# Performance work log

Measured on AMD Instinct MI355X. Metric: run time of the kernel, lower is better.

Reference implementation:

```python
import jax, jax.numpy as jnp
import numpy as np

BITS = 4
GROUP_SIZE = 128
IN_FEATURES = 4096
OUT_FEATURES = 14336
M = 256  # rows of x; >= kernel_switch_threshold so torch takes the dequant+matmul path


def setup_inputs() -> dict:
    key = jax.random.key(0)
    k1, k2, k3, k4 = jax.random.split(key, 4)
    x = jax.random.normal(k1, (M, IN_FEATURES), dtype=jnp.float16)
    # packed int4 weights: in_features//32*bits rows of int32
    qweight = jax.random.randint(
        k2, (IN_FEATURES // 32 * BITS, OUT_FEATURES), 0, 2**31 - 1, dtype=jnp.int32
    )
    n_groups = IN_FEATURES // GROUP_SIZE
    scales = jax.random.uniform(k3, (n_groups, OUT_FEATURES), dtype=jnp.float32) * 0.01 + 0.001
    # note: module stores zeros as scale*zero product (see pack()); any float works
    zeros = jax.random.uniform(k4, (n_groups, OUT_FEATURES), dtype=jnp.float32) * 0.05
    return {"x": x, "qweight": qweight, "scales": scales, "zeros": zeros}


def reference(x, qweight, scales, zeros):
    # Unpack 8 int4 values from each int32 (little-endian nibbles), matching
    # torch: (qweight[:,None,:] >> wf) & 0xF with wf = [0,4,...,28].
    shifts = jnp.arange(0, 32, BITS, dtype=jnp.int32)          # [8]
    w = (qweight[:, None, :] >> shifts[None, :, None]) & (2**BITS - 1)  # [K/8, 8, N]
    w = w.reshape(-1, GROUP_SIZE, qweight.shape[1])             # [n_groups, group, N]
    s = scales.astype(jnp.float16)[:, None, :]                  # [n_groups, 1, N]
    z = zeros.astype(jnp.float16)[:, None, :]
    # group-wise asymmetric dequant: scale * q - (scale*zero)
    w = (s * w.astype(jnp.float16) - z).reshape(-1, qweight.shape[1])  # [K, N]
    out = jnp.matmul(x, w)                                      # [M, N] fp16
    return out.astype(x.dtype)
```

## Files before the change

### kernel.cpp

```cpp
#include <hip/hip_runtime.h>
#include <hip/hip_fp16.h>

typedef unsigned int u32;
typedef unsigned short u16;
typedef __attribute__((ext_vector_type(8))) _Float16 f16x8;
typedef __attribute__((ext_vector_type(4))) float f32x4;
typedef __attribute__((ext_vector_type(4))) u32 u32x4;

#define M_DIM 256
#define K_DIM 4096
#define N_DIM 14336
#define BM 64
#define BN 128
#define BK 64
#define KHALF (K_DIM / 2)
#define NITER (KHALF / BK)
#define NBLK 896
#define LDA 72

union U4F8 { u32x4 u; f16x8 v; };

__device__ __forceinline__ f16x8 dq8(u32 q, __half2 s2, __half2 d2, __half2 z2) {
  const u32 q1 = q >> 4, q2 = q >> 8, q3 = q >> 12;
  U4F8 r;
  const u32 x0 = ( q & 0x000F000Fu) | 0x64006400u;
  const u32 x1 = (q1 & 0x000F000Fu) | 0x64006400u;
  const u32 x2 = (q2 & 0x000F000Fu) | 0x64006400u;
  const u32 x3 = (q3 & 0x000F000Fu) | 0x64006400u;
  r.u.x = __builtin_bit_cast(u32, __hsub2(__hfma2(__builtin_bit_cast(__half2, x0), s2, d2), z2));
  r.u.y = __builtin_bit_cast(u32, __hsub2(__hfma2(__builtin_bit_cast(__half2, x1), s2, d2), z2));
  r.u.z = __builtin_bit_cast(u32, __hsub2(__hfma2(__builtin_bit_cast(__half2, x2), s2, d2), z2));
  r.u.w = __builtin_bit_cast(u32, __hsub2(__hfma2(__builtin_bit_cast(__half2, x3), s2, d2), z2));
  return r.v;
}

__device__ __forceinline__ u32 pkrtz(float a, float b) {
  return __builtin_bit_cast(u32, __builtin_amdgcn_cvt_pkrtz(a, b));
}

__global__ void zero_out(float* __restrict__ O) {
  const size_t i = (size_t)blockIdx.x * 256 + threadIdx.x;
  ((f32x4*)O)[i] = (f32x4){0.f, 0.f, 0.f, 0.f};
}

__global__ __launch_bounds__(256, 3) void kivi_gemm(
    const float* __restrict__ X,
    const int* __restrict__ QW,
    const float* __restrict__ S,
    const float* __restrict__ Z,
    float* __restrict__ O)
{
  __shared__ __align__(16) u16 As[2][BM][LDA];

  const int tid  = threadIdx.x;
  const int lane = tid & 63;
  const int wn   = tid >> 6;

  const int b   = blockIdx.x;
  const int L   = (b & 7) * 112 + (b >> 3);
  const int kh  = L / 448;
  const int rem = L % 448;
  const int nt  = rem >> 2;
  const int mt  = rem & 3;
  const int m0  = mt * BM;
  const int n0  = nt * BN;
  const int kb  = kh * KHALF;
  const int kb8 = kh * (KHALF / 8);

  const int fr = lane & 15, fq = lane >> 4;
  const int cb = n0 + wn * 32 + fr;

  const int arow = tid >> 2;
  const int aseg = (tid & 3) * 16;

  f32x4 acc[4][2];
#pragma unroll
  for (int mi = 0; mi < 4; ++mi)
#pragma unroll
    for (int ni = 0; ni < 2; ++ni)
      acc[mi][ni] = (f32x4){0.f, 0.f, 0.f, 0.f};

  f32x4 aR[4];
  u32 q0[2][2], q1[2][2], q2[2][2], q3[2][2];
  float s0[2], z0[2], s1[2], z1[2], s2[2], z2[2], s3[2], z3[2];

  auto loadAx = [&](int t) {
    const float* p = X + (size_t)(m0 + arow) * K_DIM + kb + t * BK + aseg;
    aR[0] = *(const f32x4*)(p);
    aR[1] = *(const f32x4*)(p + 4);
    aR[2] = *(const f32x4*)(p + 8);
    aR[3] = *(const f32x4*)(p + 12);
  };
  auto writeAx = [&](int buf) {
#pragma unroll
    for (int c = 0; c < 2; ++c) {
      u32x4 pk;
      pk.x = pkrtz(aR[c * 2][0], aR[c * 2 + 1][0]);
      pk.y = pkrtz(aR[c * 2][1], aR[c * 2 + 1][1]);
      pk.z = pkrtz(aR[c * 2][2], aR[c * 2 + 1][2]);
      pk.w = pkrtz(aR[c * 2][3], aR[c * 2 + 1][3]);
      *(u32x4*)&As[buf][arow][aseg + c * 8] = pk;
    }
  };
  auto loadBq = [&](int t, u32 (&q)[2][2], float (&s)[2], float (&z)[2]) {
    const size_t rbase = (size_t)(kb8 + t * 8 + fq) * N_DIM + cb;
#pragma unroll
    for (int ks = 0; ks < 2; ++ks)
#pragma unroll
      for (int ni = 0; ni < 2; ++ni)
        q[ks][ni] = *(const u32*)(QW + rbase + (size_t)ks * 4 * N_DIM + ni * 16);
    const int g = kh * 16 + (t >> 1);
#pragma unroll
    for (int ni = 0; ni < 2; ++ni) {
      s[ni] = S[(size_t)g * N_DIM + cb + ni * 16];
      z[ni] = Z[(size_t)g * N_DIM + cb + ni * 16];
    }
  };
  auto computeT = [&](int buf, const u32 (&q)[2][2],
                      const float (&s)[2], const float (&z)[2]) {
    const __half hneg1024 = __float2half(-1024.f);
    __half2 sh2[2], dh2[2], zh2[2];
#pragma unroll
    for (int ni = 0; ni < 2; ++ni) {
      const __half sh = __float2half(s[ni]);
      const __half zh = __float2half(z[ni]);
      const __half dh = __hmul(sh, hneg1024);
      sh2[ni] = __halves2half2(sh, sh);
      dh2[ni] = __halves2half2(dh, dh);
      zh2[ni] = __halves2half2(zh, zh);
    }
#pragma unroll
    for (int ks = 0; ks < 2; ++ks) {
      f16x8 af[4], bf[2];
#pragma unroll
      for (int mi = 0; mi < 4; ++mi)
        af[mi] = *(const f16x8*)&As[buf][mi * 16 + fr][ks * 32 + fq * 8];
#pragma unroll
      for (int ni = 0; ni < 2; ++ni)
        bf[ni] = dq8(q[ks][ni], sh2[ni], dh2[ni], zh2[ni]);
#pragma unroll
      for (int mi = 0; mi < 4; ++mi)
#pragma unroll
        for (int ni = 0; ni < 2; ++ni)
          acc[mi][ni] = __builtin_amdgcn_mfma_f32_16x16x32_f16(
              af[mi], bf[ni], acc[mi][ni], 0, 0, 0);
    }
  };

#define LGKM_BARRIER() do {                                    \
    asm volatile("s_waitcnt lgkmcnt(0)" ::: "memory");         \
    __builtin_amdgcn_s_barrier();                              \
  } while (0)

  loadAx(0);
  loadBq(0, q0, s0, z0);
  loadBq(1, q1, s1, z1);
  writeAx(0);
  LGKM_BARRIER();

#pragma unroll 1
  for (int tb = 0; tb < NITER; tb += 4) {
    loadAx(tb + 1);
    loadBq(tb + 2, q2, s2, z2);
    __builtin_amdgcn_sched_barrier(0);
    computeT(0, q0, s0, z0);
    writeAx(1);
    LGKM_BARRIER();

    loadAx(tb + 2);
    loadBq(tb + 3, q3, s3, z3);
    __builtin_amdgcn_sched_barrier(0);
    computeT(1, q1, s1, z1);
    writeAx(0);
    LGKM_BARRIER();

    loadAx(tb + 3);
    if (tb + 4 < NITER) loadBq(tb + 4, q0, s0, z0);
    __builtin_amdgcn_sched_barrier(0);
    computeT(0, q2, s2, z2);
    writeAx(1);
    LGKM_BARRIER();

    if (tb + 4 < NITER) loadAx(tb + 4);
    if (tb + 5 < NITER) loadBq(tb + 5, q1, s1, z1);
    __builtin_amdgcn_sched_barrier(0);
    computeT(1, q3, s3, z3);
    if (tb + 4 < NITER) writeAx(0);
    LGKM_BARRIER();
  }
#undef LGKM_BARRIER

#pragma unroll
  for (int mi = 0; mi < 4; ++mi)
#pragma unroll
    for (int ni = 0; ni < 2; ++ni)
#pragma unroll
      for (int r = 0; r < 4; ++r) {
        const int row = m0 + mi * 16 + fq * 4 + r;
        const int col = n0 + wn * 32 + ni * 16 + fr;
        atomicAdd(&O[(size_t)row * N_DIM + col], acc[mi][ni][r]);
      }
}

extern "C" void kernel_launch(void* const* d_in, const int* in_sizes, int n_in,
                              void* d_out, int out_size, void* d_ws, size_t ws_size,
                              hipStream_t stream) {
  const float* X  = (const float*)d_in[0];
  const int*   QW = (const int*)d_in[1];
  const float* S  = (const float*)d_in[2];
  const float* Zp = (const float*)d_in[3];
  float* O = (float*)d_out;
  hipLaunchKernelGGL(zero_out, dim3(3584), dim3(256), 0, stream, O);
  hipLaunchKernelGGL(kivi_gemm, dim3(NBLK), dim3(256), 0, stream, X, QW, S, Zp, O);
}
```

Before: 65.76 us.

## Drop split-K and atomics, use smaller 32x64 tiles with swizzled LDS

Replaces the split-K scheme (two K halves accumulated with fp32 atomics after a separate zeroing kernel) with full-K blocks of 32x64 outputs and 128 threads, so each output is written once with a plain store. This removes the zero-fill launch and the atomic read-modify-write traffic. It also adds an XOR swizzle on the LDS A tile to avoid bank conflicts, and raises wave priority around the MFMA sequence. The trade-off is that each int4 weight tile is now loaded and dequantized by twice as many M-tiles, which doubles weight traffic and dequant ALU work.

```diff
diff --git a/kernel.cpp b/kernel.cpp
--- a/kernel.cpp
+++ b/kernel.cpp
@@ -10,13 +10,11 @@
 #define M_DIM 256
 #define K_DIM 4096
 #define N_DIM 14336
-#define BM 64
-#define BN 128
+#define BM 32
+#define BN 64
 #define BK 64
-#define KHALF (K_DIM / 2)
-#define NITER (KHALF / BK)
-#define NBLK 896
-#define LDA 72
+#define NT (K_DIM / BK)
+#define NBLK 1792
 
 union U4F8 { u32x4 u; f16x8 v; };
 
@@ -38,44 +36,37 @@
   return __builtin_bit_cast(u32, __builtin_amdgcn_cvt_pkrtz(a, b));
 }
 
-__global__ void zero_out(float* __restrict__ O) {
-  const size_t i = (size_t)blockIdx.x * 256 + threadIdx.x;
-  ((f32x4*)O)[i] = (f32x4){0.f, 0.f, 0.f, 0.f};
-}
-
-__global__ __launch_bounds__(256, 3) void kivi_gemm(
+__global__ __launch_bounds__(128, 4) void kivi_gemm(
     const float* __restrict__ X,
     const int* __restrict__ QW,
     const float* __restrict__ S,
     const float* __restrict__ Z,
     float* __restrict__ O)
 {
-  __shared__ __align__(16) u16 As[2][BM][LDA];
+  __shared__ __align__(16) u16 As[2][BM][64];
 
   const int tid  = threadIdx.x;
   const int lane = tid & 63;
   const int wn   = tid >> 6;
 
-  const int b   = blockIdx.x;
-  const int L   = (b & 7) * 112 + (b >> 3);
-  const int kh  = L / 448;
-  const int rem = L % 448;
-  const int nt  = rem >> 2;
-  const int mt  = rem & 3;
-  const int m0  = mt * BM;
-  const int n0  = nt * BN;
-  const int kb  = kh * KHALF;
-  const int kb8 = kh * (KHALF / 8);
+  const int b  = blockIdx.x;
+  const int L  = (b & 7) * 224 + (b >> 3);
+  const int nt = L >> 3;
+  const int mt = L & 7;
+  const int m0 = mt * BM;
+  const int n0 = nt * BN;
 
   const int fr = lane & 15, fq = lane >> 4;
   const int cb = n0 + wn * 32 + fr;
 
   const int arow = tid >> 2;
-  const int aseg = (tid & 3) * 16;
+  const int acol = (tid & 3) * 16;
+  const int awz  = (arow & 7) << 3;
+  const int rwz  = (fr & 7) << 3;
 
-  f32x4 acc[4][2];
+  f32x4 acc[2][2];
 #pragma unroll
-  for (int mi = 0; mi < 4; ++mi)
+  for (int mi = 0; mi < 2; ++mi)
 #pragma unroll
     for (int ni = 0; ni < 2; ++ni)
       acc[mi][ni] = (f32x4){0.f, 0.f, 0.f, 0.f};
@@ -85,7 +76,7 @@
   float s0[2], z0[2], s1[2], z1[2], s2[2], z2[2], s3[2], z3[2];
 
   auto loadAx = [&](int t) {
-    const float* p = X + (size_t)(m0 + arow) * K_DIM + kb + t * BK + aseg;
+    const float* p = X + (size_t)(m0 + arow) * K_DIM + t * BK + acol;
     aR[0] = *(const f32x4*)(p);
     aR[1] = *(const f32x4*)(p + 4);
     aR[2] = *(const f32x4*)(p + 8);
@@ -99,17 +90,17 @@
       pk.y = pkrtz(aR[c * 2][1], aR[c * 2 + 1][1]);
       pk.z = pkrtz(aR[c * 2][2], aR[c * 2 + 1][2]);
       pk.w = pkrtz(aR[c * 2][3], aR[c * 2 + 1][3]);
-      *(u32x4*)&As[buf][arow][aseg + c * 8] = pk;
+      *(u32x4*)&As[buf][arow][(acol + c * 8) ^ awz] = pk;
     }
   };
   auto loadBq = [&](int t, u32 (&q)[2][2], float (&s)[2], float (&z)[2]) {
-    const size_t rbase = (size_t)(kb8 + t * 8 + fq) * N_DIM + cb;
+    const size_t rbase = (size_t)(t * 8 + fq) * N_DIM + cb;
 #pragma unroll
     for (int ks = 0; ks < 2; ++ks)
 #pragma unroll
       for (int ni = 0; ni < 2; ++ni)
         q[ks][ni] = *(const u32*)(QW + rbase + (size_t)ks * 4 * N_DIM + ni * 16);
-    const int g = kh * 16 + (t >> 1);
+    const int g = t >> 1;
 #pragma unroll
     for (int ni = 0; ni < 2; ++ni) {
       s[ni] = S[(size_t)g * N_DIM + cb + ni * 16];
@@ -131,74 +122,59 @@
     }
 #pragma unroll
     for (int ks = 0; ks < 2; ++ks) {
-      f16x8 af[4], bf[2];
+      f16x8 af[2], bf[2];
 #pragma unroll
-      for (int mi = 0; mi < 4; ++mi)
-        af[mi] = *(const f16x8*)&As[buf][mi * 16 + fr][ks * 32 + fq * 8];
+      for (int mi = 0; mi < 2; ++mi)
+        af[mi] = *(const f16x8*)&As[buf][mi * 16 + fr][(ks * 32 + fq * 8) ^ rwz];
 #pragma unroll
       for (int ni = 0; ni < 2; ++ni)
         bf[ni] = dq8(q[ks][ni], sh2[ni], dh2[ni], zh2[ni]);
+      __builtin_amdgcn_s_setprio(1);
 #pragma unroll
-      for (int mi = 0; mi < 4; ++mi)
+      for (int mi = 0; mi < 2; ++mi)
 #pragma unroll
         for (int ni = 0; ni < 2; ++ni)
           acc[mi][ni] = __builtin_amdgcn_mfma_f32_16x16x32_f16(
               af[mi], bf[ni], acc[mi][ni], 0, 0, 0);
+      __builtin_amdgcn_s_setprio(0);
     }
   };
 
-#define LGKM_BARRIER() do {                                    \
-    asm volatile("s_waitcnt lgkmcnt(0)" ::: "memory");         \
-    __builtin_amdgcn_s_barrier();                              \
-  } while (0)
+#define PHASE(T, QC, SC, ZC, QN, SN, ZN, CUR) {            \
+    if ((T) + 1 < NT) loadAx((T) + 1);                     \
+    if ((T) + 2 < NT) loadBq((T) + 2, QN, SN, ZN);         \
+    __builtin_amdgcn_sched_barrier(0);                     \
+    computeT((CUR), QC, SC, ZC);                           \
+    if ((T) + 1 < NT) writeAx((CUR) ^ 1);                  \
+    asm volatile("s_waitcnt lgkmcnt(0)" ::: "memory");     \
+    __builtin_amdgcn_s_barrier();                          \
+  }
 
   loadAx(0);
   loadBq(0, q0, s0, z0);
   loadBq(1, q1, s1, z1);
   writeAx(0);
-  LGKM_BARRIER();
+  asm volatile("s_waitcnt lgkmcnt(0)" ::: "memory");
+  __builtin_amdgcn_s_barrier();
 
 #pragma unroll 1
-  for (int tb = 0; tb < NITER; tb += 4) {
-    loadAx(tb + 1);
-    loadBq(tb + 2, q2, s2, z2);
-    __builtin_amdgcn_sched_barrier(0);
-    computeT(0, q0, s0, z0);
-    writeAx(1);
-    LGKM_BARRIER();
-
-    loadAx(tb + 2);
-    loadBq(tb + 3, q3, s3, z3);
-    __builtin_amdgcn_sched_barrier(0);
-    computeT(1, q1, s1, z1);
-    writeAx(0);
-    LGKM_BARRIER();
-
-    loadAx(tb + 3);
-    if (tb + 4 < NITER) loadBq(tb + 4, q0, s0, z0);
-    __builtin_amdgcn_sched_barrier(0);
-    computeT(0, q2, s2, z2);
-    writeAx(1);
-    LGKM_BARRIER();
-
-    if (tb + 4 < NITER) loadAx(tb + 4);
-    if (tb + 5 < NITER) loadBq(tb + 5, q1, s1, z1);
-    __builtin_amdgcn_sched_barrier(0);
-    computeT(1, q3, s3, z3);
-    if (tb + 4 < NITER) writeAx(0);
-    LGKM_BARRIER();
+  for (int tb = 0; tb < NT; tb += 4) {
+    PHASE(tb + 0, q0, s0, z0, q2, s2, z2, 0);
+    PHASE(tb + 1, q1, s1, z1, q3, s3, z3, 1);
+    PHASE(tb + 2, q2, s2, z2, q0, s0, z0, 0);
+    PHASE(tb + 3, q3, s3, z3, q1, s1, z1, 1);
   }
-#undef LGKM_BARRIER
+#undef PHASE
 
 #pragma unroll
-  for (int mi = 0; mi < 4; ++mi)
+  for (int mi = 0; mi < 2; ++mi)
 #pragma unroll
     for (int ni = 0; ni < 2; ++ni)
 #pragma unroll
       for (int r = 0; r < 4; ++r) {
         const int row = m0 + mi * 16 + fq * 4 + r;
         const int col = n0 + wn * 32 + ni * 16 + fr;
-        atomicAdd(&O[(size_t)row * N_DIM + col], acc[mi][ni][r]);
+        O[(size_t)row * N_DIM + col] = acc[mi][ni][r];
       }
 }
 
@@ -210,6 +186,5 @@
   const float* S  = (const float*)d_in[2];
   const float* Zp = (const float*)d_in[3];
   float* O = (float*)d_out;
-  hipLaunchKernelGGL(zero_out, dim3(3584), dim3(256), 0, stream, O);
-  hipLaunchKernelGGL(kivi_gemm, dim3(NBLK), dim3(256), 0, stream, X, QW, S, Zp, O);
+  hipLaunchKernelGGL(kivi_gemm, dim3(NBLK), dim3(128), 0, stream, X, QW, S, Zp, O);
 }
```

Result: slower. 77.30 us (+17.6%).
